# Performance work log

Measured on AMD Instinct MI355X. Metric: run time of the kernel, lower is better.

## Reference

```python
import jax, jax.numpy as jnp
import numpy as np

N = 100000   # nodes in batched graph
E = 1600000  # edges (before self-loops)
D = 128      # in_dim == hidden_dim == num_outputs
G = 64       # graphs in the batch


def setup_inputs() -> dict:
    key = jax.random.key(0)
    ks = jax.random.split(key, 8)
    s = 1.0 / np.sqrt(D)
    x = jax.random.normal(ks[0], (N, D), jnp.float32)
    src = jax.random.randint(ks[1], (E,), 0, N, dtype=jnp.int64)
    dst = jax.random.randint(ks[2], (E,), 0, N, dtype=jnp.int64)
    graph_ids = jnp.sort(jax.random.randint(ks[3], (N,), 0, G, dtype=jnp.int64))
    W0 = jax.random.normal(ks[4], (D, D), jnp.float32) * s
    W1 = jax.random.normal(ks[5], (D, D), jnp.float32) * s
    W2 = jax.random.normal(ks[6], (D, D), jnp.float32) * s
    b0 = jnp.zeros((D,), jnp.float32)
    b1 = jnp.zeros((D,), jnp.float32)
    b2 = jnp.zeros((D,), jnp.float32)
    return {"x": x, "W0": W0, "b0": b0, "W1": W1, "b1": b1,
            "W2": W2, "b2": b2, "src": src, "dst": dst, "graph_ids": graph_ids}


def reference(x, W0, b0, W1, b1, W2, b2, src, dst, graph_ids):
    n = x.shape[0]
    loops = jnp.arange(n, dtype=src.dtype)
    src_f = jnp.concatenate([src, loops])  # add self-loops once (dgl.add_self_loop)
    dst_f = jnp.concatenate([dst, loops])
    ones_e = jnp.ones(src_f.shape, x.dtype)
    deg_out = jax.ops.segment_sum(ones_e, src_f, num_segments=n)  # >=1 (self-loop)
    deg_in = jax.ops.segment_sum(ones_e, dst_f, num_segments=n)
    cs = jax.lax.rsqrt(deg_out)[:, None]  # source norm (GraphConv norm='both')
    cd = jax.lax.rsqrt(deg_in)[:, None]   # destination norm

    def gcn_layer(h, W, b):
        m = (h * cs)[src_f]                                   # [E+N, D] gather
        agg = jax.ops.segment_sum(m, dst_f, num_segments=n)   # scatter-add SpMM
        return jax.nn.relu((agg * cd) @ W + b)                # F.relu(conv(g, h))

    h = gcn_layer(x, W0, b0)
    h = gcn_layer(h, W1, b1)
    h = gcn_layer(h, W2, b2)

    # dgl.mean_nodes: per-graph mean over nodes
    sums = jax.ops.segment_sum(h, graph_ids, num_segments=G)
    cnt = jax.ops.segment_sum(jnp.ones((n, 1), h.dtype), graph_ids, num_segments=G)
    return sums / jnp.maximum(cnt, 1.0)  # [G, D] logits
```

## Files before the change

### kernel.cpp

```cpp
#include <hip/hip_runtime.h>
#include <stdint.h>

#define D 128
#define CAP 64
#define HB 128
#define CH 25000

typedef __attribute__((ext_vector_type(8))) short bf16x8;
typedef __attribute__((ext_vector_type(4))) float f32x4;

__device__ inline unsigned short f2bf(float x) {
  union { float f; uint32_t u; } v; v.f = x;
  uint32_t u = v.u;
  u += 0x7fffu + ((u >> 16) & 1u);
  return (unsigned short)(u >> 16);
}
__device__ inline float bflo(uint32_t u) {
  union { uint32_t u; float f; } v; v.u = u << 16; return v.f;
}
__device__ inline float bfhi(uint32_t u) {
  union { uint32_t u; float f; } v; v.u = u & 0xffff0000u; return v.f;
}
__device__ inline uint32_t packbf(float lo, float hi) {
  return (uint32_t)f2bf(lo) | ((uint32_t)f2bf(hi) << 16);
}

__global__ __launch_bounds__(256) void hist_kernel(
    const int* __restrict__ src, const int* __restrict__ dst,
    unsigned int* __restrict__ parts_s, unsigned int* __restrict__ parts_d,
    int E, int N,
    const float* __restrict__ W0, const float* __restrict__ W1,
    const float* __restrict__ W2, unsigned short* __restrict__ Wt,
    int* __restrict__ cnt, int G, float* __restrict__ outz, int out_total) {
  __shared__ unsigned int lbs[CH / 8];
  __shared__ unsigned int lbd[CH / 8];
  int b = blockIdx.x & (HB - 1);
  int lo = (blockIdx.x >> 7) * CH;
  for (int i = threadIdx.x; i < CH / 8; i += 256) { lbs[i] = 0; lbd[i] = 0; }
  __syncthreads();
  int per = (E + HB - 1) / HB;
  int e0 = b * per;
  int e1 = min(e0 + per, E);
  for (int e = e0 + threadIdx.x; e < e1; e += 256) {
    int rs = src[e] - lo;
    if ((unsigned)rs < CH) atomicAdd(&lbs[rs >> 3], 1u << ((rs & 7) * 4));
    int rd = dst[e] - lo;
    if ((unsigned)rd < CH) atomicAdd(&lbd[rd >> 3], 1u << ((rd & 7) * 4));
  }
  __syncthreads();
  int nu = (N + 7) / 8;
  int base = lo >> 3;
  int cu = min(CH / 8, nu - base);
  unsigned int* ps = parts_s + (size_t)b * nu + base;
  unsigned int* pd = parts_d + (size_t)b * nu + base;
  for (int i = threadIdx.x; i < cu; i += 256) { ps[i] = lbs[i]; pd[i] = lbd[i]; }

  int gs = gridDim.x * 256;
  for (int i = blockIdx.x * 256 + threadIdx.x; i < 3 * 16384; i += gs) {
    int l = i >> 14, r = i & 16383;
    int n = r >> 7, k = r & 127;
    const float* W = (l == 0) ? W0 : (l == 1) ? W1 : W2;
    Wt[i] = f2bf(W[k * 128 + n]);
  }
  for (int i = blockIdx.x * 256 + threadIdx.x; i < G; i += gs) cnt[i] = 0;
  for (int i = blockIdx.x * 256 + threadIdx.x; i < out_total; i += gs) outz[i] = 0.f;
}

__global__ __launch_bounds__(256) void scan_norm_kernel(
    const unsigned char* __restrict__ parts_s,
    const unsigned char* __restrict__ parts_d,
    unsigned char* __restrict__ offs_d,
    int* __restrict__ degd,
    float* __restrict__ cs, float* __restrict__ cd,
    const int* __restrict__ gid, int* __restrict__ cnt,
    int N, int G) {
  __shared__ int lcnt[256];
  for (int i = threadIdx.x; i < G; i += 256) lcnt[i] = 0;
  __syncthreads();

  int t = blockIdx.x * blockDim.x + threadIdx.x;
  int i0 = t * 2;
  if (i0 < N) {
    int nb = N / 2;
    int ds0 = 0, ds1 = 0, dd0 = 0, dd1 = 0;
    for (int bb = 0; bb < HB; bb += 16) {
      unsigned char svv[16], dvv[16];
#pragma unroll
      for (int k = 0; k < 16; k++) {
        svv[k] = parts_s[(size_t)(bb + k) * nb + t];
        dvv[k] = parts_d[(size_t)(bb + k) * nb + t];
      }
#pragma unroll
      for (int k = 0; k < 16; k++) {
        ds0 += svv[k] & 15; ds1 += svv[k] >> 4;
        offs_d[(size_t)(bb + k) * N + i0]     = (unsigned char)min(dd0, 255);
        offs_d[(size_t)(bb + k) * N + i0 + 1] = (unsigned char)min(dd1, 255);
        dd0 += dvv[k] & 15; dd1 += dvv[k] >> 4;
      }
    }
    degd[i0] = dd0;     degd[i0 + 1] = dd1;
    cs[i0] = rsqrtf((float)ds0 + 1.0f);
    cs[i0 + 1] = rsqrtf((float)ds1 + 1.0f);
    cd[i0] = rsqrtf((float)dd0 + 1.0f);
    cd[i0 + 1] = rsqrtf((float)dd1 + 1.0f);
    atomicAdd(&lcnt[gid[i0]], 1);
    if (i0 + 1 < N) atomicAdd(&lcnt[gid[i0 + 1]], 1);
  }
  __syncthreads();
  for (int i = threadIdx.x; i < G; i += 256) {
    int c = lcnt[i];
    if (c) atomicAdd(&cnt[i], c);
  }
}

__global__ __launch_bounds__(256) void fill_kernel(
    const int* __restrict__ src, const int* __restrict__ dst,
    const unsigned char* __restrict__ offs_d, int* __restrict__ col, int E, int N,
    const float* __restrict__ x, const float* __restrict__ cs,
    uint32_t* __restrict__ xs) {
  __shared__ unsigned int lcur[CH / 8];
  int b = blockIdx.x & (HB - 1);
  int lo = (blockIdx.x >> 7) * CH;
  for (int i = threadIdx.x; i < CH / 8; i += 256) lcur[i] = 0;
  __syncthreads();
  int per = (E + HB - 1) / HB;
  int e0 = b * per;
  int e1 = min(e0 + per, E);
  const unsigned char* offb = offs_d + (size_t)b * N;
  int e = e0 + threadIdx.x;
  for (; e + 768 < e1; e += 1024) {
    int dd4[4], ss4[4], rd4[4];
    unsigned char ob4[4];
#pragma unroll
    for (int k = 0; k < 4; k++) { dd4[k] = dst[e + k * 256]; ss4[k] = src[e + k * 256]; }
#pragma unroll
    for (int k = 0; k < 4; k++) {
      rd4[k] = dd4[k] - lo;
      ob4[k] = ((unsigned)rd4[k] < CH) ? offb[dd4[k]] : (unsigned char)0;
    }
#pragma unroll
    for (int k = 0; k < 4; k++) {
      if ((unsigned)rd4[k] < CH) {
        unsigned old = atomicAdd(&lcur[rd4[k] >> 3], 1u << ((rd4[k] & 7) * 4));
        int local = (old >> ((rd4[k] & 7) * 4)) & 0xF;
        int pos = (int)ob4[k] + local;
        if (pos < CAP) col[(size_t)dd4[k] * CAP + pos] = ss4[k];
      }
    }
  }
  for (; e < e1; e += 256) {
    int d = dst[e];
    int rd = d - lo;
    if ((unsigned)rd < CH) {
      unsigned old = atomicAdd(&lcur[rd >> 3], 1u << ((rd & 7) * 4));
      int local = (old >> ((rd & 7) * 4)) & 0xF;
      int pos = (int)offb[d] + local;
      if (pos < CAP) col[(size_t)d * CAP + pos] = src[e];
    }
  }
  int total4 = N * 32;
  int gs = gridDim.x * 256;
  for (int i = blockIdx.x * 256 + threadIdx.x; i < total4; i += gs) {
    float4 v = ((const float4*)x)[i];
    float c = cs[i >> 5];
    uint2 o;
    o.x = packbf(v.x * c, v.y * c);
    o.y = packbf(v.z * c, v.w * c);
    ((uint2*)xs)[i] = o;
  }
}

__global__ __launch_bounds__(512) void fused_layer_kernel(
    const uint32_t* __restrict__ hin, const unsigned short* __restrict__ Wt,
    const float* __restrict__ bias, const float* __restrict__ cd,
    const float* __restrict__ rowscale, const int* __restrict__ degd,
    const int* __restrict__ col, unsigned short* __restrict__ hout, int N) {
  __shared__ __align__(16) uint32_t At[16 * 68];

  int wv = threadIdx.x >> 6;
  int lane = threadIdx.x & 63;
  int m = lane & 15;
  int quad = lane >> 4;

  bf16x8 bfr[4];
#pragma unroll
  for (int c = 0; c < 4; c++)
    bfr[c] = *(const bf16x8*)(Wt + (size_t)(16 * wv + m) * 128 + c * 32 + quad * 8);

#pragma unroll
  for (int j = 0; j < 2; j++) {
    int w = __builtin_amdgcn_readfirstlane(blockIdx.x * 16 + wv * 2 + j);
    float accx = 0.f, accy = 0.f;
    if (w < N) {
      int n = min(degd[w], CAP);
      const int* cw = col + (size_t)w * CAP;
      const uint32_t* hl = hin + lane;
      uint32_t selfv = hl[(size_t)w * 64];
      accx = bflo(selfv); accy = bfhi(selfv);
      int i = 0;
      for (; i + 7 < n; i += 8) {
        int s0 = cw[i],     s1 = cw[i + 1], s2 = cw[i + 2], s3 = cw[i + 3];
        int s4 = cw[i + 4], s5 = cw[i + 5], s6 = cw[i + 6], s7 = cw[i + 7];
        uint32_t v0 = hl[(size_t)s0 * 64];
        uint32_t v1 = hl[(size_t)s1 * 64];
        uint32_t v2 = hl[(size_t)s2 * 64];
        uint32_t v3 = hl[(size_t)s3 * 64];
        uint32_t v4 = hl[(size_t)s4 * 64];
        uint32_t v5 = hl[(size_t)s5 * 64];
        uint32_t v6 = hl[(size_t)s6 * 64];
        uint32_t v7 = hl[(size_t)s7 * 64];
        accx += bflo(v0); accy += bfhi(v0);
        accx += bflo(v1); accy += bfhi(v1);
        accx += bflo(v2); accy += bfhi(v2);
        accx += bflo(v3); accy += bfhi(v3);
        accx += bflo(v4); accy += bfhi(v4);
        accx += bflo(v5); accy += bfhi(v5);
        accx += bflo(v6); accy += bfhi(v6);
        accx += bflo(v7); accy += bfhi(v7);
      }
      for (; i + 3 < n; i += 4) {
        int s0 = cw[i], s1 = cw[i + 1], s2 = cw[i + 2], s3 = cw[i + 3];
        uint32_t v0 = hl[(size_t)s0 * 64];
        uint32_t v1 = hl[(size_t)s1 * 64];
        uint32_t v2 = hl[(size_t)s2 * 64];
        uint32_t v3 = hl[(size_t)s3 * 64];
        accx += bflo(v0); accy += bfhi(v0);
        accx += bflo(v1); accy += bfhi(v1);
        accx += bflo(v2); accy += bfhi(v2);
        accx += bflo(v3); accy += bfhi(v3);
      }
      for (; i < n; i++) {
        uint32_t v = hl[(size_t)cw[i] * 64];
        accx += bflo(v); accy += bfhi(v);
      }
      float cdv = cd[w];
      accx *= cdv; accy *= cdv;
    }
    At[(wv * 2 + j) * 68 + lane] = packbf(accx, accy);
  }
  __syncthreads();

  const unsigned short* arow = (const unsigned short*)At + m * 136;
  f32x4 acc = f32x4{0.f, 0.f, 0.f, 0.f};
#pragma unroll
  for (int c = 0; c < 4; c++) {
    bf16x8 a = *(const bf16x8*)(arow + c * 32 + quad * 8);
    acc = __builtin_amdgcn_mfma_f32_16x16x32_bf16(a, bfr[c], acc, 0, 0, 0);
  }
  int colb = 16 * wv + m;
  float bv = bias[colb];
#pragma unroll
  for (int i = 0; i < 4; i++) {
    int r = blockIdx.x * 16 + quad * 4 + i;
    if (r < N) {
      float v = acc[i] + bv;
      v = v > 0.f ? v : 0.f;
      if (rowscale) v *= rowscale[r];
      hout[(size_t)r * D + colb] = f2bf(v);
    }
  }
}

__global__ void pool_kernel(const unsigned short* __restrict__ h, const int* __restrict__ gid,
                            float* __restrict__ outsum, const int* __restrict__ cnt, int N) {
  int v0 = blockIdx.x * 64;
  if (v0 >= N) return;
  int d = threadIdx.x;
  int vend = min(v0 + 64, N);
  int cur = gid[v0];
  float acc = 0.f;
  for (int v = v0; v < vend; v++) {
    int g = gid[v];
    if (g != cur) {
      float inv = 1.0f / fmaxf((float)cnt[cur], 1.0f);
      atomicAdd(&outsum[cur * D + d], acc * inv);
      acc = 0.f; cur = g;
    }
    unsigned short hv = __builtin_nontemporal_load(&h[(size_t)v * D + d]);
    union { uint32_t u; float f; } cv; cv.u = (uint32_t)hv << 16;
    acc += cv.f;
  }
  float inv = 1.0f / fmaxf((float)cnt[cur], 1.0f);
  atomicAdd(&outsum[cur * D + d], acc * inv);
}

extern "C" void kernel_launch(void* const* d_in, const int* in_sizes, int n_in,
                              void* d_out, int out_size, void* d_ws, size_t ws_size,
                              hipStream_t stream) {
  const float* x  = (const float*)d_in[0];
  const float* W0 = (const float*)d_in[1];
  const float* b0 = (const float*)d_in[2];
  const float* W1 = (const float*)d_in[3];
  const float* b1 = (const float*)d_in[4];
  const float* W2 = (const float*)d_in[5];
  const float* b2 = (const float*)d_in[6];
  const int* src  = (const int*)d_in[7];
  const int* dst  = (const int*)d_in[8];
  const int* gid  = (const int*)d_in[9];

  const int N = in_sizes[0] / D;
  const int E = in_sizes[7];
  const int G = out_size / D;
  const int nu = (N + 7) / 8;

  uint32_t* hsA = (uint32_t*)d_ws;
  uint32_t* hsB = hsA + (size_t)N * 64;
  int* col      = (int*)(hsB + (size_t)N * 64);
  int* degd     = col + (size_t)N * CAP;
  float* csb    = (float*)(degd + N);
  float* cdb    = csb + N;
  int* cnt      = (int*)(cdb + N);
  unsigned short* Wt = (unsigned short*)(cnt + G);
  unsigned int* parts_s = (unsigned int*)(Wt + 3 * 16384);
  unsigned int* parts_d = parts_s + (size_t)HB * nu;
  unsigned char* offs_d = (unsigned char*)(parts_d + (size_t)HB * nu);

  const int nch = (N + CH - 1) / CH;
  hist_kernel<<<HB * nch, 256, 0, stream>>>(src, dst, parts_s, parts_d, E, N,
                                            W0, W1, W2, Wt, cnt, G,
                                            (float*)d_out, out_size);
  scan_norm_kernel<<<(N / 2 + 255) / 256, 256, 0, stream>>>(
      (const unsigned char*)parts_s, (const unsigned char*)parts_d, offs_d,
      degd, csb, cdb, gid, cnt, N, G);
  fill_kernel<<<HB * nch, 256, 0, stream>>>(src, dst, offs_d, col, E, N, x, csb, hsA);

  const int ltiles = (N + 15) / 16;

  fused_layer_kernel<<<ltiles, 512, 0, stream>>>(hsA, Wt, b0, cdb, csb, degd, col,
                                                 (unsigned short*)hsB, N);
  fused_layer_kernel<<<ltiles, 512, 0, stream>>>(hsB, Wt + 16384, b1, cdb, csb, degd, col,
                                                 (unsigned short*)hsA, N);
  fused_layer_kernel<<<ltiles, 512, 0, stream>>>(hsA, Wt + 2 * 16384, b2, cdb, nullptr, degd, col,
                                                 (unsigned short*)hsB, N);

  pool_kernel<<<(N + 63) / 64, 128, 0, stream>>>((const unsigned short*)hsB, gid,
                                                 (float*)d_out, cnt, N);
}
```

Baseline: 433.4 us.

## Fuse mean-pool into last GCN layer and enlarge preprocessing blocks

After: 442.6 us. +2.1%, slower.

```diff
diff --git a/kernel.cpp b/kernel.cpp
--- a/kernel.cpp
+++ b/kernel.cpp
@@ -25,7 +25,7 @@
   return (uint32_t)f2bf(lo) | ((uint32_t)f2bf(hi) << 16);
 }
 
-__global__ __launch_bounds__(256) void hist_kernel(
+__global__ __launch_bounds__(512) void hist_kernel(
     const int* __restrict__ src, const int* __restrict__ dst,
     unsigned int* __restrict__ parts_s, unsigned int* __restrict__ parts_d,
     int E, int N,
@@ -36,12 +36,12 @@
   __shared__ unsigned int lbd[CH / 8];
   int b = blockIdx.x & (HB - 1);
   int lo = (blockIdx.x >> 7) * CH;
-  for (int i = threadIdx.x; i < CH / 8; i += 256) { lbs[i] = 0; lbd[i] = 0; }
+  for (int i = threadIdx.x; i < CH / 8; i += 512) { lbs[i] = 0; lbd[i] = 0; }
   __syncthreads();
   int per = (E + HB - 1) / HB;
   int e0 = b * per;
   int e1 = min(e0 + per, E);
-  for (int e = e0 + threadIdx.x; e < e1; e += 256) {
+  for (int e = e0 + threadIdx.x; e < e1; e += 512) {
     int rs = src[e] - lo;
     if ((unsigned)rs < CH) atomicAdd(&lbs[rs >> 3], 1u << ((rs & 7) * 4));
     int rd = dst[e] - lo;
@@ -53,17 +53,17 @@
   int cu = min(CH / 8, nu - base);
   unsigned int* ps = parts_s + (size_t)b * nu + base;
   unsigned int* pd = parts_d + (size_t)b * nu + base;
-  for (int i = threadIdx.x; i < cu; i += 256) { ps[i] = lbs[i]; pd[i] = lbd[i]; }
-
-  int gs = gridDim.x * 256;
-  for (int i = blockIdx.x * 256 + threadIdx.x; i < 3 * 16384; i += gs) {
+  for (int i = threadIdx.x; i < cu; i += 512) { ps[i] = lbs[i]; pd[i] = lbd[i]; }
+
+  int gs = gridDim.x * 512;
+  for (int i = blockIdx.x * 512 + threadIdx.x; i < 3 * 16384; i += gs) {
     int l = i >> 14, r = i & 16383;
     int n = r >> 7, k = r & 127;
     const float* W = (l == 0) ? W0 : (l == 1) ? W1 : W2;
     Wt[i] = f2bf(W[k * 128 + n]);
   }
-  for (int i = blockIdx.x * 256 + threadIdx.x; i < G; i += gs) cnt[i] = 0;
-  for (int i = blockIdx.x * 256 + threadIdx.x; i < out_total; i += gs) outz[i] = 0.f;
+  for (int i = blockIdx.x * 512 + threadIdx.x; i < G; i += gs) cnt[i] = 0;
+  for (int i = blockIdx.x * 512 + threadIdx.x; i < out_total; i += gs) outz[i] = 0.f;
 }
 
 __global__ __launch_bounds__(256) void scan_norm_kernel(
@@ -78,33 +78,30 @@
   for (int i = threadIdx.x; i < G; i += 256) lcnt[i] = 0;
   __syncthreads();
 
-  int t = blockIdx.x * blockDim.x + threadIdx.x;
-  int i0 = t * 2;
-  if (i0 < N) {
+  int t = blockIdx.x * 256 + threadIdx.x;
+  if (t < N) {
     int nb = N / 2;
-    int ds0 = 0, ds1 = 0, dd0 = 0, dd1 = 0;
+    int half = t >> 1;
+    int sh = (t & 1) * 4;
+    int ds = 0, dd = 0;
     for (int bb = 0; bb < HB; bb += 16) {
       unsigned char svv[16], dvv[16];
 #pragma unroll
       for (int k = 0; k < 16; k++) {
-        svv[k] = parts_s[(size_t)(bb + k) * nb + t];
-        dvv[k] = parts_d[(size_t)(bb + k) * nb + t];
+        svv[k] = parts_s[(size_t)(bb + k) * nb + half];
+        dvv[k] = parts_d[(size_t)(bb + k) * nb + half];
       }
 #pragma unroll
       for (int k = 0; k < 16; k++) {
-        ds0 += svv[k] & 15; ds1 += svv[k] >> 4;
-        offs_d[(size_t)(bb + k) * N + i0]     = (unsigned char)min(dd0, 255);
-        offs_d[(size_t)(bb + k) * N + i0 + 1] = (unsigned char)min(dd1, 255);
-        dd0 += dvv[k] & 15; dd1 += dvv[k] >> 4;
-      }
-    }
-    degd[i0] = dd0;     degd[i0 + 1] = dd1;
-    cs[i0] = rsqrtf((float)ds0 + 1.0f);
-    cs[i0 + 1] = rsqrtf((float)ds1 + 1.0f);
-    cd[i0] = rsqrtf((float)dd0 + 1.0f);
-    cd[i0 + 1] = rsqrtf((float)dd1 + 1.0f);
-    atomicAdd(&lcnt[gid[i0]], 1);
-    if (i0 + 1 < N) atomicAdd(&lcnt[gid[i0 + 1]], 1);
+        ds += (svv[k] >> sh) & 15;
+        offs_d[(size_t)(bb + k) * N + t] = (unsigned char)min(dd, 255);
+        dd += (dvv[k] >> sh) & 15;
+      }
+    }
+    degd[t] = dd;
+    cs[t] = rsqrtf((float)ds + 1.0f);
+    cd[t] = rsqrtf((float)dd + 1.0f);
+    atomicAdd(&lcnt[gid[t]], 1);
   }
   __syncthreads();
   for (int i = threadIdx.x; i < G; i += 256) {
@@ -113,7 +110,7 @@
   }
 }
 
-__global__ __launch_bounds__(256) void fill_kernel(
+__global__ __launch_bounds__(512) void fill_kernel(
     const int* __restrict__ src, const int* __restrict__ dst,
     const unsigned char* __restrict__ offs_d, int* __restrict__ col, int E, int N,
     const float* __restrict__ x, const float* __restrict__ cs,
@@ -121,18 +118,18 @@
   __shared__ unsigned int lcur[CH / 8];
   int b = blockIdx.x & (HB - 1);
   int lo = (blockIdx.x >> 7) * CH;
-  for (int i = threadIdx.x; i < CH / 8; i += 256) lcur[i] = 0;
+  for (int i = threadIdx.x; i < CH / 8; i += 512) lcur[i] = 0;
   __syncthreads();
   int per = (E + HB - 1) / HB;
   int e0 = b * per;
   int e1 = min(e0 + per, E);
   const unsigned char* offb = offs_d + (size_t)b * N;
   int e = e0 + threadIdx.x;
-  for (; e + 768 < e1; e += 1024) {
+  for (; e + 1536 < e1; e += 2048) {
     int dd4[4], ss4[4], rd4[4];
     unsigned char ob4[4];
 #pragma unroll
-    for (int k = 0; k < 4; k++) { dd4[k] = dst[e + k * 256]; ss4[k] = src[e + k * 256]; }
+    for (int k = 0; k < 4; k++) { dd4[k] = dst[e + k * 512]; ss4[k] = src[e + k * 512]; }
 #pragma unroll
     for (int k = 0; k < 4; k++) {
       rd4[k] = dd4[k] - lo;
@@ -148,7 +145,7 @@
       }
     }
   }
-  for (; e < e1; e += 256) {
+  for (; e < e1; e += 512) {
     int d = dst[e];
     int rd = d - lo;
     if ((unsigned)rd < CH) {
@@ -159,13 +156,13 @@
     }
   }
   int total4 = N * 32;
-  int gs = gridDim.x * 256;
-  for (int i = blockIdx.x * 256 + threadIdx.x; i < total4; i += gs) {
+  int gs = gridDim.x * 512;
+  for (int i = blockIdx.x * 512 + threadIdx.x; i < total4; i += gs) {
     float4 v = ((const float4*)x)[i];
-    float c = cs[i >> 5];
+    float cc = cs[i >> 5];
     uint2 o;
-    o.x = packbf(v.x * c, v.y * c);
-    o.y = packbf(v.z * c, v.w * c);
+    o.x = packbf(v.x * cc, v.y * cc);
+    o.y = packbf(v.z * cc, v.w * cc);
     ((uint2*)xs)[i] = o;
   }
 }
@@ -174,13 +171,18 @@
     const uint32_t* __restrict__ hin, const unsigned short* __restrict__ Wt,
     const float* __restrict__ bias, const float* __restrict__ cd,
     const float* __restrict__ rowscale, const int* __restrict__ degd,
-    const int* __restrict__ col, unsigned short* __restrict__ hout, int N) {
+    const int* __restrict__ col, unsigned short* __restrict__ hout, int N,
+    const int* __restrict__ gidp, const int* __restrict__ cntp,
+    float* __restrict__ outsum) {
   __shared__ __align__(16) uint32_t At[16 * 68];
+  __shared__ float ldsacc[4 * 128];
 
   int wv = threadIdx.x >> 6;
   int lane = threadIdx.x & 63;
   int m = lane & 15;
   int quad = lane >> 4;
+
+  if (outsum) ldsacc[threadIdx.x] = 0.f;
 
   bf16x8 bfr[4];
 #pragma unroll
@@ -249,39 +251,47 @@
   }
   int colb = 16 * wv + m;
   float bv = bias[colb];
-#pragma unroll
-  for (int i = 0; i < 4; i++) {
-    int r = blockIdx.x * 16 + quad * 4 + i;
-    if (r < N) {
-      float v = acc[i] + bv;
-      v = v > 0.f ? v : 0.f;
-      if (rowscale) v *= rowscale[r];
-      hout[(size_t)r * D + colb] = f2bf(v);
-    }
-  }
-}
-
-__global__ void pool_kernel(const unsigned short* __restrict__ h, const int* __restrict__ gid,
-                            float* __restrict__ outsum, const int* __restrict__ cnt, int N) {
-  int v0 = blockIdx.x * 64;
-  if (v0 >= N) return;
-  int d = threadIdx.x;
-  int vend = min(v0 + 64, N);
-  int cur = gid[v0];
-  float acc = 0.f;
-  for (int v = v0; v < vend; v++) {
-    int g = gid[v];
-    if (g != cur) {
-      float inv = 1.0f / fmaxf((float)cnt[cur], 1.0f);
-      atomicAdd(&outsum[cur * D + d], acc * inv);
-      acc = 0.f; cur = g;
-    }
-    unsigned short hv = __builtin_nontemporal_load(&h[(size_t)v * D + d]);
-    union { uint32_t u; float f; } cv; cv.u = (uint32_t)hv << 16;
-    acc += cv.f;
-  }
-  float inv = 1.0f / fmaxf((float)cnt[cur], 1.0f);
-  atomicAdd(&outsum[cur * D + d], acc * inv);
+  if (outsum == nullptr) {
+#pragma unroll
+    for (int i = 0; i < 4; i++) {
+      int r = blockIdx.x * 16 + quad * 4 + i;
+      if (r < N) {
+        float v = acc[i] + bv;
+        v = v > 0.f ? v : 0.f;
+        if (rowscale) v *= rowscale[r];
+        hout[(size_t)r * D + colb] = f2bf(v);
+      }
+    }
+  } else {
+    int r0 = blockIdx.x * 16;
+    int g_lo = gidp[min(r0, N - 1)];
+    int g_hi = gidp[min(r0 + 15, N - 1)];
+    int span = g_hi - g_lo + 1;
+#pragma unroll
+    for (int i = 0; i < 4; i++) {
+      int r = r0 + quad * 4 + i;
+      if (r < N) {
+        float v = acc[i] + bv;
+        v = v > 0.f ? v : 0.f;
+        int g = gidp[r];
+        if (span <= 4) {
+          atomicAdd(&ldsacc[(g - g_lo) * 128 + colb], v);
+        } else {
+          atomicAdd(&outsum[g * D + colb], v / fmaxf((float)cntp[g], 1.0f));
+        }
+      }
+    }
+    __syncthreads();
+    if (span <= 4) {
+      int gg = threadIdx.x >> 7, c = threadIdx.x & 127;
+      if (gg < span) {
+        float s = ldsacc[threadIdx.x];
+        if (s != 0.f)
+          atomicAdd(&outsum[(g_lo + gg) * D + c],
+                    s / fmaxf((float)cntp[g_lo + gg], 1.0f));
+      }
+    }
+  }
 }
 
 extern "C" void kernel_launch(void* const* d_in, const int* in_sizes, int n_in,
@@ -316,23 +326,23 @@
   unsigned char* offs_d = (unsigned char*)(parts_d + (size_t)HB * nu);
 
   const int nch = (N + CH - 1) / CH;
-  hist_kernel<<<HB * nch, 256, 0, stream>>>(src, dst, parts_s, parts_d, E, N,
+  hist_kernel<<<HB * nch, 512, 0, stream>>>(src, dst, parts_s, parts_d, E, N,
                                             W0, W1, W2, Wt, cnt, G,
                                             (float*)d_out, out_size);
-  scan_norm_kernel<<<(N / 2 + 255) / 256, 256, 0, stream>>>(
+  scan_norm_kernel<<<(N + 255) / 256, 256, 0, stream>>>(
       (const unsigned char*)parts_s, (const unsigned char*)parts_d, offs_d,
       degd, csb, cdb, gid, cnt, N, G);
-  fill_kernel<<<HB * nch, 256, 0, stream>>>(src, dst, offs_d, col, E, N, x, csb, hsA);
+  fill_kernel<<<HB * nch, 512, 0, stream>>>(src, dst, offs_d, col, E, N, x, csb, hsA);
 
   const int ltiles = (N + 15) / 16;
 
   fused_layer_kernel<<<ltiles, 512, 0, stream>>>(hsA, Wt, b0, cdb, csb, degd, col,
-                                                 (unsigned short*)hsB, N);
+                                                 (unsigned short*)hsB, N,
+                                                 nullptr, nullptr, nullptr);
   fused_layer_kernel<<<ltiles, 512, 0, stream>>>(hsB, Wt + 16384, b1, cdb, csb, degd, col,
-                                                 (unsigned short*)hsA, N);
+                                                 (unsigned short*)hsA, N,
+                                                 nullptr, nullptr, nullptr);
   fused_layer_kernel<<<ltiles, 512, 0, stream>>>(hsA, Wt + 2 * 16384, b2, cdb, nullptr, degd, col,
-                                                 (unsigned short*)hsB, N);
-
-  pool_kernel<<<(N + 63) / 64, 128, 0, stream>>>((const unsigned short*)hsB, gid,
-                                                 (float*)d_out, cnt, N);
-}
+                                                 (unsigned short*)hsB, N,
+                                                 gid, cnt, (float*)d_out);
+}
```
